# Kernel optimization log

Measured on AMD Instinct MI355X. Metric: run time of the kernel, lower is better.

Reference implementation:

```python
import jax, jax.numpy as jnp
import numpy as np

HIDDEN = 1024
NUM_HEADS = 16
HEAD_DIM = HIDDEN // NUM_HEADS
LN_EPS = 1e-12


def setup_inputs() -> dict:
    key = jax.random.key(0)
    ks = jax.random.split(key, 12)
    B, S, H = 4, 2048, HIDDEN
    scale = 0.02
    return {
        "hidden_states": jax.random.normal(ks[0], (B, S, H), dtype=jnp.float32),
        "attention_mask": jnp.zeros((B, 1, 1, S), dtype=jnp.float32),
        "Wq": jax.random.normal(ks[1], (H, H), dtype=jnp.float32) * scale,
        "bq": jnp.zeros((H,), dtype=jnp.float32),
        "Wk": jax.random.normal(ks[2], (H, H), dtype=jnp.float32) * scale,
        "bk": jnp.zeros((H,), dtype=jnp.float32),
        "Wv": jax.random.normal(ks[3], (H, H), dtype=jnp.float32) * scale,
        "bv": jnp.zeros((H,), dtype=jnp.float32),
        "Wo": jax.random.normal(ks[4], (H, H), dtype=jnp.float32) * scale,
        "bo": jnp.zeros((H,), dtype=jnp.float32),
        "ln_gamma": jnp.ones((H,), dtype=jnp.float32),
        "ln_beta": jnp.zeros((H,), dtype=jnp.float32),
    }


def _split_heads(x):  # [B,S,H] -> [B,nh,S,hd]
    B, S, _ = x.shape
    return x.reshape(B, S, NUM_HEADS, HEAD_DIM).transpose(0, 2, 1, 3)


def reference(hidden_states, attention_mask, Wq, bq, Wk, bk, Wv, bv, Wo, bo, ln_gamma, ln_beta):
    # QKV projections (torch Linear: x @ W.T + b)
    q = _split_heads(hidden_states @ Wq.T + bq)
    k = _split_heads(hidden_states @ Wk.T + bk)
    v = _split_heads(hidden_states @ Wv.T + bv)
    # scaled dot-product attention with additive mask (dropout=identity, eval)
    scores = jnp.einsum('bhqd,bhkd->bhqk', q, k) / jnp.sqrt(jnp.float32(HEAD_DIM))
    scores = scores + attention_mask
    probs = jax.nn.softmax(scores, axis=-1)
    ctx = jnp.einsum('bhqk,bhkd->bhqd', probs, v)
    B, _, S, _ = ctx.shape
    ctx = ctx.transpose(0, 2, 1, 3).reshape(B, S, HIDDEN)
    # output projection + residual + LayerNorm
    out = ctx @ Wo.T + bo + hidden_states
    mu = jnp.mean(out, axis=-1, keepdims=True)
    var = jnp.mean(jnp.square(out - mu), axis=-1, keepdims=True)
    return (out - mu) * jax.lax.rsqrt(var + LN_EPS) * ln_gamma + ln_beta
```

## Files before the change

### kernel.cpp

```cpp
#include <hip/hip_runtime.h>
#include <stdint.h>

#define SEQ   2048
#define BATCH 4
#define NH    16
#define HD    64
#define H     1024
#define QKVN  3072

typedef unsigned short u16;
typedef unsigned int   u32;
typedef __bf16 bf16x8 __attribute__((ext_vector_type(8)));
typedef float  f32x4  __attribute__((ext_vector_type(4)));
typedef float  f32x16 __attribute__((ext_vector_type(16)));
typedef unsigned int v2u   __attribute__((ext_vector_type(2)));
typedef unsigned int u32x4 __attribute__((ext_vector_type(4)));

#define MFMA16(a, b, c) __builtin_amdgcn_mfma_f32_16x16x32_bf16((a), (b), (c), 0, 0, 0)
#define MFMA32(a, b, c) __builtin_amdgcn_mfma_f32_32x32x16_bf16((a), (b), (c), 0, 0, 0)
#define LOG2E 1.4426950408889634f
#define SC    (0.125f * LOG2E)

__device__ __forceinline__ u16 f2bf(float f) {
  u32 u = __float_as_uint(f);
  u = (u + 0x7fffu + ((u >> 16) & 1u)) >> 16;
  return (u16)u;
}

__device__ __forceinline__ void gload16(const u16* g, u16* l) {
  __builtin_amdgcn_global_load_lds(
      (const __attribute__((address_space(1))) u32*)g,
      (__attribute__((address_space(3))) u32*)l, 16, 0, 0);
}

__device__ __forceinline__ u32 lds_addr(const void* p) {
  return (u32)(uintptr_t)(const __attribute__((address_space(3))) void*)p;
}

__device__ __forceinline__ u32 cvtpk(float lo, float hi) {
  u32 r;
  asm("v_cvt_pk_bf16_f32 %0, %1, %2" : "=v"(r) : "v"(lo), "v"(hi));
  return r;
}

__global__ __launch_bounds__(256) void cast_all(
    const float* __restrict__ hid, const float* __restrict__ wq,
    const float* __restrict__ wk,  const float* __restrict__ wv,
    const float* __restrict__ wo,
    u16* __restrict__ hb, u16* __restrict__ wqkv, u16* __restrict__ wo_b)
{
  int i = blockIdx.x * 256 + threadIdx.x;
  const float* s; u16* d; int idx;
  if (i < 2097152) { s = hid; d = hb; idx = i; }
  else {
    int j = i - 2097152;
    int w = j >> 18; idx = j & 262143;
    if      (w == 0) { s = wq; d = wqkv; }
    else if (w == 1) { s = wk; d = wqkv + 1048576; }
    else if (w == 2) { s = wv; d = wqkv + 2097152; }
    else             { s = wo; d = wo_b; }
  }
  float4 v = ((const float4*)s)[idx];
  ushort4 o;
  o.x = f2bf(v.x); o.y = f2bf(v.y); o.z = f2bf(v.z); o.w = f2bf(v.w);
  ((ushort4*)d)[idx] = o;
}

template<int EPI>
__global__ __launch_bounds__(256, 2) void gemm_bf16(
    const u16* __restrict__ A, const u16* __restrict__ B,
    u16* __restrict__ outb, float* __restrict__ outf, int ldc,
    const float* __restrict__ b0, const float* __restrict__ b1,
    const float* __restrict__ b2, const float* __restrict__ resid)
{
  __shared__ __align__(16) u16 As[128 * 32];
  __shared__ __align__(16) u16 Bs[128 * 32];
  const int tid = threadIdx.x;
  const int lane = tid & 63;
  const int wv = tid >> 6, wr = wv >> 1, wc = wv & 1;
  const int l15 = lane & 15, l4 = lane >> 4;

  const int nwg = gridDim.x * gridDim.y;
  const int flat = blockIdx.y * gridDim.x + blockIdx.x;
  const int swz = (flat & 7) * (nwg >> 3) + (flat >> 3);
  const int row0 = (swz / gridDim.x) * 128, col0 = (swz % gridDim.x) * 128;

  const f32x4 fz = {0.f, 0.f, 0.f, 0.f};
  f32x4 acc[4][4];
#pragma unroll
  for (int i = 0; i < 4; ++i)
#pragma unroll
    for (int j = 0; j < 4; ++j) acc[i][j] = fz;

  const int srow = lane >> 2;
  const int skol = (lane & 3) * 8;
  const u16* Ab = A + (size_t)(row0 + srow) * 1024 + skol;
  const u16* Bb = B + (size_t)(col0 + srow) * 1024 + skol;
  const int c0 = wv * 2;

  for (int kt = 0; kt < 1024; kt += 32) {
    gload16(Ab + (size_t)(c0 * 16) * 1024 + kt,       &As[(c0 * 16) * 32]);
    gload16(Ab + (size_t)(c0 * 16 + 16) * 1024 + kt,  &As[(c0 * 16 + 16) * 32]);
    gload16(Bb + (size_t)(c0 * 16) * 1024 + kt,       &Bs[(c0 * 16) * 32]);
    gload16(Bb + (size_t)(c0 * 16 + 16) * 1024 + kt,  &Bs[(c0 * 16 + 16) * 32]);
    __syncthreads();

    bf16x8 af[4], bfr[4];
#pragma unroll
    for (int f = 0; f < 4; ++f) {
      af[f]  = *(const bf16x8*)&As[(wr * 64 + f * 16 + l15) * 32 + l4 * 8];
      bfr[f] = *(const bf16x8*)&Bs[(wc * 64 + f * 16 + l15) * 32 + l4 * 8];
    }
#pragma unroll
    for (int i = 0; i < 4; ++i)
#pragma unroll
      for (int j = 0; j < 4; ++j)
        acc[i][j] = MFMA16(af[i], bfr[j], acc[i][j]);
    __syncthreads();
  }

  if (EPI == 0) {
    const float* bias = (col0 < 1024) ? b0 : (col0 < 2048) ? b1 : b2;
#pragma unroll
    for (int i = 0; i < 4; ++i) {
      int gr0 = row0 + wr * 64 + i * 16 + l4 * 4;
#pragma unroll
      for (int j = 0; j < 4; ++j) {
        int gc = col0 + wc * 64 + j * 16 + l15;
        float bv = bias[gc & 1023];
#pragma unroll
        for (int r = 0; r < 4; ++r)
          outb[(size_t)(gr0 + r) * ldc + gc] = f2bf(acc[i][j][r] + bv);
      }
    }
  } else {
#pragma unroll
    for (int i = 0; i < 4; ++i) {
      int gr0 = row0 + wr * 64 + i * 16 + l4 * 4;
#pragma unroll
      for (int j = 0; j < 4; ++j) {
        int gc = col0 + wc * 64 + j * 16 + l15;
        float bv = b0[gc];
#pragma unroll
        for (int r = 0; r < 4; ++r) {
          size_t idx = (size_t)(gr0 + r) * ldc + gc;
          outf[idx] = acc[i][j][r] + bv + resid[idx];
        }
      }
    }
  }
}

__global__ __launch_bounds__(256, 2) void flash_attn(
    const u16* __restrict__ qkv, const float* __restrict__ mask,
    u16* __restrict__ ctxb)
{
  __shared__ __align__(16) u16 Qs[128 * 64];
  __shared__ __align__(16) u16 Ks[64 * 64];
  __shared__ __align__(16) u16 Vs[4096];

  const int flat = (blockIdx.z * 16 + blockIdx.y) * 16 + blockIdx.x;
  const int swzb = (flat & 7) * 128 + (flat >> 3);
  const int qt = swzb & 15, h = (swzb >> 4) & 15, b = swzb >> 8;

  const int tid = threadIdx.x, lane = tid & 63, wq = tid >> 6;
  const int l31 = lane & 31, l15 = lane & 15, h5 = lane >> 5;

  const size_t tokb = (size_t)b * SEQ;
  const u16* Qg = qkv + (tokb + (size_t)qt * 128) * QKVN + h * HD;
  const u16* Kg = qkv + tokb * QKVN + 1024 + h * HD;
  const u16* Vg = qkv + tokb * QKVN + 2048 + h * HD;
  const float* maskp = mask + (size_t)b * SEQ;

#pragma unroll
  for (int cc = 0; cc < 4; ++cc) {
    int c = tid + cc * 256;
    int r = c >> 3, ko = (c & 7) * 8;
    u32 qb = (u32)(r * 128 + ko * 2) ^ ((r & 7) << 4);
    *(uint4*)((char*)Qs + qb) = *(const uint4*)&Qg[(size_t)r * QKVN + ko];
  }
  __syncthreads();

  const u32 swzl = (u32)((l31 & 7) << 4);
  u32 cb[4];
#pragma unroll
  for (int kb = 0; kb < 4; ++kb)
    cb[kb] = ((u32)(kb * 32 + h5 * 16)) ^ swzl;

  bf16x8 qf[4];
#pragma unroll
  for (int kb = 0; kb < 4; ++kb)
    qf[kb] = *(const bf16x8*)((char*)Qs + (u32)((wq * 32 + l31) * 128) + cb[kb]);

  float m_run = -1e30f, l_run = 0.f;
  f32x16 ctx0 = {}, ctx1 = {};

  const int sr = tid >> 3, sk = (tid & 7) * 8;
  const u32 kwb0 = ((u32)(sr * 128 + sk * 2)) ^ ((sr & 7) << 4);
  const u32 kwb1 = ((u32)((sr + 32) * 128 + sk * 2)) ^ ((sr & 7) << 4);
  const u32 vw0 = (u32)((sk >> 4) * 1024 + (sr >> 2) * 64 + (sr & 3) * 16 + (sk & 15));
  const u32 vw1 = (u32)((sk >> 4) * 1024 + ((sr + 32) >> 2) * 64 + (sr & 3) * 16 + (sk & 15));

  const u32 vaddr = lds_addr(Vs) + (u32)(l15 * 8 + ((lane >> 4) & 1) * 2048 + h5 * 256);

  uint4 kr0 = *(const uint4*)&Kg[(size_t)sr * QKVN + sk];
  uint4 kr1 = *(const uint4*)&Kg[(size_t)(sr + 32) * QKVN + sk];
  uint4 vr0 = *(const uint4*)&Vg[(size_t)sr * QKVN + sk];
  uint4 vr1 = *(const uint4*)&Vg[(size_t)(sr + 32) * QKVN + sk];

  for (int kv0 = 0; kv0 < SEQ; kv0 += 64) {
    *(uint4*)((char*)Ks + kwb0) = kr0;
    *(uint4*)((char*)Ks + kwb1) = kr1;
    *(uint4*)&Vs[vw0] = vr0;
    *(uint4*)&Vs[vw1] = vr1;
    __syncthreads();

    if (kv0 + 64 < SEQ) {
      kr0 = *(const uint4*)&Kg[(size_t)(kv0 + 64 + sr) * QKVN + sk];
      kr1 = *(const uint4*)&Kg[(size_t)(kv0 + 96 + sr) * QKVN + sk];
      vr0 = *(const uint4*)&Vg[(size_t)(kv0 + 64 + sr) * QKVN + sk];
      vr1 = *(const uint4*)&Vg[(size_t)(kv0 + 96 + sr) * QKVN + sk];
    }

    f32x16 s0 = {}, s1 = {};
    __builtin_amdgcn_s_setprio(1);
#pragma unroll
    for (int kb = 0; kb < 4; ++kb) {
      bf16x8 a0 = *(const bf16x8*)((char*)Ks + (u32)(l31 * 128) + cb[kb]);
      bf16x8 a1 = *(const bf16x8*)((char*)Ks + (u32)(l31 * 128 + 4096) + cb[kb]);
      s0 = MFMA32(a0, qf[kb], s0);
      s1 = MFMA32(a1, qf[kb], s1);
    }
    __builtin_amdgcn_s_setprio(0);

#pragma unroll
    for (int r = 0; r < 16; ++r) {
      int kvr = kv0 + (r & 3) + 8 * (r >> 2);
      float ma = maskp[kvr],      mb = maskp[kvr + 4];
      float mc = maskp[kvr + 32], md = maskp[kvr + 36];
      float mv0 = (h5 ? mb : ma) * LOG2E;
      float mv1 = (h5 ? md : mc) * LOG2E;
      s0[r] = s0[r] * SC + mv0;
      s1[r] = s1[r] * SC + mv1;
    }

    float mx = s0[0];
#pragma unroll
    for (int r = 1; r < 16; ++r) mx = fmaxf(mx, s0[r]);
#pragma unroll
    for (int r = 0; r < 16; ++r) mx = fmaxf(mx, s1[r]);
    mx = fmaxf(mx, __shfl_xor(mx, 32));

    bool need = (mx > m_run + 11.5415603f);
    if (__any((int)need)) {
      float mn = fmaxf(m_run, mx);
      float al = exp2f(m_run - mn);
      m_run = mn;
      l_run *= al;
#pragma unroll
      for (int r = 0; r < 16; ++r) {
        float av = __shfl(al, (r & 3) + 8 * (r >> 2) + 4 * h5);
        ctx0[r] *= av;
        ctx1[r] *= av;
      }
    }

    float ps = 0.f;
#pragma unroll
    for (int r = 0; r < 16; ++r) { s0[r] = exp2f(s0[r] - m_run); ps += s0[r]; }
#pragma unroll
    for (int r = 0; r < 16; ++r) { s1[r] = exp2f(s1[r] - m_run); ps += s1[r]; }
    ps += __shfl_xor(ps, 32);
    l_run += ps;

    bf16x8 paf[4];
#pragma unroll
    for (int blk = 0; blk < 4; ++blk) {
      u32 w0, w1, w2, w3;
      if (blk < 2) {
        int r0 = blk * 8;
        w0 = cvtpk(s0[r0 + 0], s0[r0 + 1]); w1 = cvtpk(s0[r0 + 2], s0[r0 + 3]);
        w2 = cvtpk(s0[r0 + 4], s0[r0 + 5]); w3 = cvtpk(s0[r0 + 6], s0[r0 + 7]);
      } else {
        int r0 = (blk - 2) * 8;
        w0 = cvtpk(s1[r0 + 0], s1[r0 + 1]); w1 = cvtpk(s1[r0 + 2], s1[r0 + 3]);
        w2 = cvtpk(s1[r0 + 4], s1[r0 + 5]); w3 = cvtpk(s1[r0 + 6], s1[r0 + 7]);
      }
      asm volatile("v_permlane32_swap_b32 %0, %1" : "+v"(w0), "+v"(w2));
      asm volatile("v_permlane32_swap_b32 %0, %1" : "+v"(w1), "+v"(w3));
      u32x4 ww = {w0, w1, w2, w3};
      paf[blk] = __builtin_bit_cast(bf16x8, ww);
    }

    __builtin_amdgcn_s_setprio(1);
#pragma unroll
    for (int db = 0; db < 2; ++db) {
      v2u t[8];
#pragma unroll
      for (int kb = 0; kb < 4; ++kb) {
        asm volatile("ds_read_b64_tr_b16 %0, %1 offset:%c2"
                     : "=&v"(t[kb * 2])     : "v"(vaddr), "i"(db * 4096 + kb * 512));
        asm volatile("ds_read_b64_tr_b16 %0, %1 offset:%c2"
                     : "=&v"(t[kb * 2 + 1]) : "v"(vaddr), "i"(db * 4096 + kb * 512 + 128));
      }
      asm volatile("s_waitcnt lgkmcnt(0)");
      __builtin_amdgcn_sched_barrier(0);
#pragma unroll
      for (int kb = 0; kb < 4; ++kb) {
        u32x4 ww = {t[kb * 2][0], t[kb * 2][1], t[kb * 2 + 1][0], t[kb * 2 + 1][1]};
        bf16x8 vf = __builtin_bit_cast(bf16x8, ww);
        if (db == 0) ctx0 = MFMA32(paf[kb], vf, ctx0);
        else         ctx1 = MFMA32(paf[kb], vf, ctx1);
      }
    }
    __builtin_amdgcn_s_setprio(0);
    __syncthreads();
  }

  float linv = 1.0f / l_run;
#pragma unroll
  for (int r = 0; r < 16; ++r) {
    int qidx = (r & 3) + 8 * (r >> 2) + 4 * h5;
    float li = __shfl(linv, qidx);
    int gr = qt * 128 + wq * 32 + qidx;
    u16* o = &ctxb[(tokb + gr) * (size_t)H + h * HD + l31];
    o[0]  = f2bf(ctx0[r] * li);
    o[32] = f2bf(ctx1[r] * li);
  }
}

__global__ __launch_bounds__(256) void ln_res(const float* __restrict__ x,
    const float* __restrict__ gamma, const float* __restrict__ beta,
    float* __restrict__ out)
{
  const int row = blockIdx.x, t = threadIdx.x;
  float4 v = ((const float4*)(x + (size_t)row * H))[t];
  float s1 = v.x + v.y + v.z + v.w;
  float s2 = v.x * v.x + v.y * v.y + v.z * v.z + v.w * v.w;
#pragma unroll
  for (int d = 1; d < 64; d <<= 1) { s1 += __shfl_xor(s1, d); s2 += __shfl_xor(s2, d); }
  __shared__ float a1[4], a2[4];
  if ((t & 63) == 0) { a1[t >> 6] = s1; a2[t >> 6] = s2; }
  __syncthreads();
  s1 = a1[0] + a1[1] + a1[2] + a1[3];
  s2 = a2[0] + a2[1] + a2[2] + a2[3];
  float mu  = s1 * (1.f / H);
  float var = s2 * (1.f / H) - mu * mu;
  float rstd = rsqrtf(var + 1e-12f);
  float4 g  = ((const float4*)gamma)[t];
  float4 be = ((const float4*)beta)[t];
  float4 o;
  o.x = (v.x - mu) * rstd * g.x + be.x;
  o.y = (v.y - mu) * rstd * g.y + be.y;
  o.z = (v.z - mu) * rstd * g.z + be.z;
  o.w = (v.w - mu) * rstd * g.w + be.w;
  ((float4*)(out + (size_t)row * H))[t] = o;
}

extern "C" void kernel_launch(void* const* d_in, const int* in_sizes, int n_in,
                              void* d_out, int out_size, void* d_ws, size_t ws_size,
                              hipStream_t stream)
{
  const float* hid  = (const float*)d_in[0];
  const float* mask = (const float*)d_in[1];
  const float* Wq   = (const float*)d_in[2];
  const float* bq   = (const float*)d_in[3];
  const float* Wk   = (const float*)d_in[4];
  const float* bk   = (const float*)d_in[5];
  const float* Wv   = (const float*)d_in[6];
  const float* bv   = (const float*)d_in[7];
  const float* Wo   = (const float*)d_in[8];
  const float* bo   = (const float*)d_in[9];
  const float* gam  = (const float*)d_in[10];
  const float* bet  = (const float*)d_in[11];

  char* ws = (char*)d_ws;
  u16*   hb   = (u16*)(ws);
  u16*   wqkv = (u16*)(ws + 16777216);
  u16*   wo_b = (u16*)(ws + 23068672);
  u16*   qkvb = (u16*)(ws + 25165824);
  u16*   ctxb = (u16*)(ws + 75497472);
  float* tmp  = (float*)(ws + 25165824);

  cast_all<<<12288, 256, 0, stream>>>(hid, Wq, Wk, Wv, Wo, hb, wqkv, wo_b);

  gemm_bf16<0><<<dim3(24, 64), 256, 0, stream>>>(hb, wqkv, qkvb, nullptr, QKVN,
                                                 bq, bk, bv, nullptr);
  flash_attn<<<dim3(16, NH, BATCH), 256, 0, stream>>>(qkvb, mask, ctxb);
  gemm_bf16<1><<<dim3(8, 64), 256, 0, stream>>>(ctxb, wo_b, nullptr, tmp, H,
                                                bo, nullptr, nullptr, hid);
  ln_res<<<8192, 256, 0, stream>>>(tmp, gam, bet, (float*)d_out);
}
```

Baseline: 361.7 us.

## Fold additive mask into V and row sums via exp(mask), compute l with MFMA

Rewrites the additive key mask as a multiplicative factor exp(mask), applied to V rows in the QKV GEMM epilogue and used as a bf16 vector whose MFMA with P gives the softmax denominator. This removes the per-element mask loads and adds from the attention inner loop, along with the scalar row-sum reduction and its cross-lane shuffle. The row max is now taken on raw scores with the scale applied afterward, via a flattened max tree. The cost is an extra MFMA per block plus a small mask-exp pass. Numerics change because the denominator is accumulated from bf16 P and mask values, and masks with large negative entries would underflow differently.

```diff
diff --git a/kernel.cpp b/kernel.cpp
--- a/kernel.cpp
+++ b/kernel.cpp
@@ -46,10 +46,23 @@
 __global__ __launch_bounds__(256) void cast_all(
     const float* __restrict__ hid, const float* __restrict__ wq,
     const float* __restrict__ wk,  const float* __restrict__ wv,
-    const float* __restrict__ wo,
-    u16* __restrict__ hb, u16* __restrict__ wqkv, u16* __restrict__ wo_b)
+    const float* __restrict__ wo,  const float* __restrict__ mask,
+    u16* __restrict__ hb, u16* __restrict__ wqkv, u16* __restrict__ wo_b,
+    float* __restrict__ mexpf, u16* __restrict__ mexpb)
 {
   int i = blockIdx.x * 256 + threadIdx.x;
+  if (i >= 3145728) {
+    int j = i - 3145728;
+    float4 mv = ((const float4*)mask)[j];
+    float4 e;
+    e.x = exp2f(mv.x * LOG2E); e.y = exp2f(mv.y * LOG2E);
+    e.z = exp2f(mv.z * LOG2E); e.w = exp2f(mv.w * LOG2E);
+    ((float4*)mexpf)[j] = e;
+    ushort4 ob;
+    ob.x = f2bf(e.x); ob.y = f2bf(e.y); ob.z = f2bf(e.z); ob.w = f2bf(e.w);
+    ((ushort4*)mexpb)[j] = ob;
+    return;
+  }
   const float* s; u16* d; int idx;
   if (i < 2097152) { s = hid; d = hb; idx = i; }
   else {
@@ -71,7 +84,8 @@
     const u16* __restrict__ A, const u16* __restrict__ B,
     u16* __restrict__ outb, float* __restrict__ outf, int ldc,
     const float* __restrict__ b0, const float* __restrict__ b1,
-    const float* __restrict__ b2, const float* __restrict__ resid)
+    const float* __restrict__ b2, const float* __restrict__ resid,
+    const float* __restrict__ mexpf)
 {
   __shared__ __align__(16) u16 As[128 * 32];
   __shared__ __align__(16) u16 Bs[128 * 32];
@@ -121,16 +135,20 @@
 
   if (EPI == 0) {
     const float* bias = (col0 < 1024) ? b0 : (col0 < 2048) ? b1 : b2;
+    const bool isv = (col0 >= 2048);
 #pragma unroll
     for (int i = 0; i < 4; ++i) {
       int gr0 = row0 + wr * 64 + i * 16 + l4 * 4;
+      float scl4[4];
+#pragma unroll
+      for (int r = 0; r < 4; ++r) scl4[r] = isv ? mexpf[gr0 + r] : 1.0f;
 #pragma unroll
       for (int j = 0; j < 4; ++j) {
         int gc = col0 + wc * 64 + j * 16 + l15;
         float bv = bias[gc & 1023];
 #pragma unroll
         for (int r = 0; r < 4; ++r)
-          outb[(size_t)(gr0 + r) * ldc + gc] = f2bf(acc[i][j][r] + bv);
+          outb[(size_t)(gr0 + r) * ldc + gc] = f2bf((acc[i][j][r] + bv) * scl4[r]);
       }
     }
   } else {
@@ -152,7 +170,7 @@
 }
 
 __global__ __launch_bounds__(256, 2) void flash_attn(
-    const u16* __restrict__ qkv, const float* __restrict__ mask,
+    const u16* __restrict__ qkv, const u16* __restrict__ mexpb,
     u16* __restrict__ ctxb)
 {
   __shared__ __align__(16) u16 Qs[128 * 64];
@@ -170,7 +188,7 @@
   const u16* Qg = qkv + (tokb + (size_t)qt * 128) * QKVN + h * HD;
   const u16* Kg = qkv + tokb * QKVN + 1024 + h * HD;
   const u16* Vg = qkv + tokb * QKVN + 2048 + h * HD;
-  const float* maskp = mask + (size_t)b * SEQ;
+  const u16* Mg = mexpb + tokb;
 
 #pragma unroll
   for (int cc = 0; cc < 4; ++cc) {
@@ -192,8 +210,8 @@
   for (int kb = 0; kb < 4; ++kb)
     qf[kb] = *(const bf16x8*)((char*)Qs + (u32)((wq * 32 + l31) * 128) + cb[kb]);
 
-  float m_run = -1e30f, l_run = 0.f;
-  f32x16 ctx0 = {}, ctx1 = {};
+  float m_run = -1e30f;
+  f32x16 ctx0 = {}, ctx1 = {}, lsum = {};
 
   const int sr = tid >> 3, sk = (tid & 7) * 8;
   const u32 kwb0 = ((u32)(sr * 128 + sk * 2)) ^ ((sr & 7) << 4);
@@ -221,6 +239,10 @@
       vr0 = *(const uint4*)&Vg[(size_t)(kv0 + 64 + sr) * QKVN + sk];
       vr1 = *(const uint4*)&Vg[(size_t)(kv0 + 96 + sr) * QKVN + sk];
     }
+    bf16x8 mf[4];
+#pragma unroll
+    for (int kb = 0; kb < 4; ++kb)
+      mf[kb] = *(const bf16x8*)&Mg[kv0 + kb * 16 + 8 * h5];
 
     f32x16 s0 = {}, s1 = {};
     __builtin_amdgcn_s_setprio(1);
@@ -233,45 +255,42 @@
     }
     __builtin_amdgcn_s_setprio(0);
 
-#pragma unroll
-    for (int r = 0; r < 16; ++r) {
-      int kvr = kv0 + (r & 3) + 8 * (r >> 2);
-      float ma = maskp[kvr],      mb = maskp[kvr + 4];
-      float mc = maskp[kvr + 32], md = maskp[kvr + 36];
-      float mv0 = (h5 ? mb : ma) * LOG2E;
-      float mv1 = (h5 ? md : mc) * LOG2E;
-      s0[r] = s0[r] * SC + mv0;
-      s1[r] = s1[r] * SC + mv1;
-    }
-
-    float mx = s0[0];
-#pragma unroll
-    for (int r = 1; r < 16; ++r) mx = fmaxf(mx, s0[r]);
-#pragma unroll
-    for (int r = 0; r < 16; ++r) mx = fmaxf(mx, s1[r]);
-    mx = fmaxf(mx, __shfl_xor(mx, 32));
-
-    bool need = (mx > m_run + 11.5415603f);
+    float t0 = fmaxf(fmaxf(s0[0],  s0[1]),  s0[2]);
+    float t1 = fmaxf(fmaxf(s0[3],  s0[4]),  s0[5]);
+    float t2 = fmaxf(fmaxf(s0[6],  s0[7]),  s0[8]);
+    float t3 = fmaxf(fmaxf(s0[9],  s0[10]), s0[11]);
+    float t4 = fmaxf(fmaxf(s0[12], s0[13]), s0[14]);
+    float t5 = fmaxf(fmaxf(s0[15], s1[0]),  s1[1]);
+    float t6 = fmaxf(fmaxf(s1[2],  s1[3]),  s1[4]);
+    float t7 = fmaxf(fmaxf(s1[5],  s1[6]),  s1[7]);
+    float t8 = fmaxf(fmaxf(s1[8],  s1[9]),  s1[10]);
+    float t9 = fmaxf(fmaxf(s1[11], s1[12]), s1[13]);
+    float ta = fmaxf(s1[14], s1[15]);
+    t0 = fmaxf(fmaxf(t0, t1), t2);
+    t3 = fmaxf(fmaxf(t3, t4), t5);
+    t6 = fmaxf(fmaxf(t6, t7), t8);
+    t9 = fmaxf(t9, ta);
+    float mxs = fmaxf(fmaxf(t0, t3), fmaxf(t6, t9)) * SC;
+    mxs = fmaxf(mxs, __shfl_xor(mxs, 32));
+
+    bool need = (mxs > m_run + 11.5415603f);
     if (__any((int)need)) {
-      float mn = fmaxf(m_run, mx);
+      float mn = fmaxf(m_run, mxs);
       float al = exp2f(m_run - mn);
       m_run = mn;
-      l_run *= al;
 #pragma unroll
       for (int r = 0; r < 16; ++r) {
         float av = __shfl(al, (r & 3) + 8 * (r >> 2) + 4 * h5);
         ctx0[r] *= av;
         ctx1[r] *= av;
-      }
-    }
-
-    float ps = 0.f;
-#pragma unroll
-    for (int r = 0; r < 16; ++r) { s0[r] = exp2f(s0[r] - m_run); ps += s0[r]; }
-#pragma unroll
-    for (int r = 0; r < 16; ++r) { s1[r] = exp2f(s1[r] - m_run); ps += s1[r]; }
-    ps += __shfl_xor(ps, 32);
-    l_run += ps;
+        lsum[r] *= av;
+      }
+    }
+
+#pragma unroll
+    for (int r = 0; r < 16; ++r) s0[r] = exp2f(s0[r] * SC - m_run);
+#pragma unroll
+    for (int r = 0; r < 16; ++r) s1[r] = exp2f(s1[r] * SC - m_run);
 
     bf16x8 paf[4];
 #pragma unroll
@@ -294,6 +313,10 @@
 
     __builtin_amdgcn_s_setprio(1);
 #pragma unroll
+    for (int kb = 0; kb < 4; ++kb)
+      lsum = MFMA32(paf[kb], mf[kb], lsum);
+
+#pragma unroll
     for (int db = 0; db < 2; ++db) {
       v2u t[8];
 #pragma unroll
@@ -317,7 +340,17 @@
     __syncthreads();
   }
 
-  float linv = 1.0f / l_run;
+  float sel = 0.f;
+  const int tt = l31 - 4 * h5;
+#pragma unroll
+  for (int r = 0; r < 16; ++r) {
+    const int c = (r & 3) + 8 * (r >> 2);
+    sel = (tt == c) ? lsum[r] : sel;
+  }
+  float pl = __shfl_xor(sel, 32);
+  float lq = (((l31 >> 2) & 1) == h5) ? sel : pl;
+  float linv = 1.0f / lq;
+
 #pragma unroll
   for (int r = 0; r < 16; ++r) {
     int qidx = (r & 3) + 8 * (r >> 2) + 4 * h5;
@@ -375,19 +408,22 @@
   const float* bet  = (const float*)d_in[11];
 
   char* ws = (char*)d_ws;
-  u16*   hb   = (u16*)(ws);
-  u16*   wqkv = (u16*)(ws + 16777216);
-  u16*   wo_b = (u16*)(ws + 23068672);
-  u16*   qkvb = (u16*)(ws + 25165824);
-  u16*   ctxb = (u16*)(ws + 75497472);
-  float* tmp  = (float*)(ws + 25165824);
-
-  cast_all<<<12288, 256, 0, stream>>>(hid, Wq, Wk, Wv, Wo, hb, wqkv, wo_b);
+  u16*   hb    = (u16*)(ws);
+  u16*   wqkv  = (u16*)(ws + 16777216);
+  u16*   wo_b  = (u16*)(ws + 23068672);
+  u16*   qkvb  = (u16*)(ws + 25165824);
+  u16*   ctxb  = (u16*)(ws + 75497472);
+  float* mexpf = (float*)(ws + 92274688);
+  u16*   mexpb = (u16*)(ws + 92307456);
+  float* tmp   = (float*)(ws + 25165824);
+
+  cast_all<<<12296, 256, 0, stream>>>(hid, Wq, Wk, Wv, Wo, mask,
+                                      hb, wqkv, wo_b, mexpf, mexpb);
 
   gemm_bf16<0><<<dim3(24, 64), 256, 0, stream>>>(hb, wqkv, qkvb, nullptr, QKVN,
-                                                 bq, bk, bv, nullptr);
-  flash_attn<<<dim3(16, NH, BATCH), 256, 0, stream>>>(qkvb, mask, ctxb);
+                                                 bq, bk, bv, nullptr, mexpf);
+  flash_attn<<<dim3(16, NH, BATCH), 256, 0, stream>>>(qkvb, mexpb, ctxb);
   gemm_bf16<1><<<dim3(8, 64), 256, 0, stream>>>(ctxb, wo_b, nullptr, tmp, H,
-                                                bo, nullptr, nullptr, hid);
+                                                bo, nullptr, nullptr, hid, nullptr);
   ln_res<<<8192, 256, 0, stream>>>(tmp, gam, bet, (float*)d_out);
 }
```

New measurement: 349.7 us. 3.3% less time.
